# Kernel optimization log

Hardware: AMD Instinct MI355X
Metric: run time of the kernel (lower is better)

The kernel has to match this reference:

```python
import jax, jax.numpy as jnp
import numpy as np

B = 16          # number of trees (batch)
H = 256         # hidden_size == feature_size
S = 16          # Tree.num_sem
C = 5           # max_child_num (complete C-ary tree)
L = 6           # tree depth: leaves at level L, internal levels 0..L-1
N_LEAF = C**L                     # 15625
N_INT = (C**L - 1) // (C - 1)     # 3906 internal nodes, level-l offset = (C^l-1)/(C-1)


def setup_inputs() -> dict:
    key = jax.random.key(0)
    ks = jax.random.split(key, 20)
    rn = lambda k, shp, s=0.05: jax.random.normal(k, shp, dtype=jnp.float32) * s
    return {
        "leaf_box": jax.random.normal(ks[0], (B, N_LEAF, 4), dtype=jnp.float32),
        "leaf_sem": jax.random.uniform(ks[1], (B, N_LEAF, S), dtype=jnp.float32),
        "internal_box": jax.random.normal(ks[2], (B, N_INT, 4), dtype=jnp.float32),
        "node_type": jax.random.randint(ks[3], (B, N_INT), 0, 3, dtype=jnp.int32),
        "eps": jax.random.normal(ks[4], (B, H), dtype=jnp.float32),
        "W_box": rn(ks[5], (4, H)), "b_box": jnp.zeros((H,), jnp.float32),
        "W_sem": rn(ks[6], (S, H)), "b_sem": jnp.zeros((H,), jnp.float32),
        "W_node": rn(ks[7], (3, C * H, H)), "b_node": jnp.zeros((3, H), jnp.float32),
        "W1": rn(ks[8], (H, H)), "b1": jnp.zeros((H,), jnp.float32),
        "Wmu": rn(ks[9], (H, H)), "bmu": jnp.zeros((H,), jnp.float32),
        "Wvar": rn(ks[10], (H, H)), "bvar": jnp.zeros((H,), jnp.float32),
    }


def reference(leaf_box, leaf_sem, internal_box, node_type, eps,
              W_box, b_box, W_sem, b_sem, W_node, b_node,
              W1, b1, Wmu, bmu, Wvar, bvar):
    box_enc = lambda b: jax.nn.relu(b @ W_box + b_box)
    # LeafEncoder: relu-box-encoding + relu-sem-encoding
    feats = box_enc(leaf_box) + jax.nn.relu(leaf_sem @ W_sem + b_sem)  # [B, N_LEAF, H]
    # Bottom-up over internal levels (static loop over L=6 levels)
    for l in range(L - 1, -1, -1):
        n = C ** l
        off = (C ** l - 1) // (C - 1)
        child = feats.reshape(B, n, C * H)  # children flattened per parent (child_exists==1)
        # Apply all 3 branch encoders (vertical/horizontal/stack), select by node label
        y_all = jnp.einsum('bnk,tkh->bnth', child, W_node) + b_node          # [B,n,3,H]
        sel = jax.nn.one_hot(node_type[:, off:off + n], 3, dtype=child.dtype)  # [B,n,3]
        y = jnp.einsum('bnth,bnt->bnh', y_all, sel)
        feats = jax.nn.relu(y) + box_enc(internal_box[:, off:off + n])
    root = feats[:, 0]  # [B, H]
    # Sampler (variational, probabilistic)
    enc = jax.nn.relu(root @ W1 + b1)
    mu = enc @ Wmu + bmu
    logvar = enc @ Wvar + bvar
    std = jnp.exp(0.5 * logvar)
    kld = 1.0 + logvar - mu ** 2 - jnp.exp(logvar)
    return jnp.concatenate([eps * std + mu, kld], axis=1)  # [B, 2H]
```

## Files before the change

### kernel.cpp

```cpp
#include <hip/hip_runtime.h>


#define B_ 16
#define H_ 256
#define NLEAF 15625
#define NINT 3906

typedef __bf16 bf16_t;
typedef bf16_t bf16x8 __attribute__((ext_vector_type(8)));
typedef bf16_t bf16x4 __attribute__((ext_vector_type(4)));
typedef float f32x4 __attribute__((ext_vector_type(4)));

__device__ __forceinline__ void gl2lds16(const bf16_t* g, bf16_t* l) {
  __builtin_amdgcn_global_load_lds((const __attribute__((address_space(1))) void*)g,
                                   (__attribute__((address_space(3))) void*)l,
                                   16, 0, 0);
}

__global__ __launch_bounds__(256) void prep_kernel(const float* __restrict__ W_node,
                                                   bf16_t* __restrict__ Wt,
                                                   int* __restrict__ counters) {
  if (blockIdx.x == 0 && threadIdx.x < 18) counters[threadIdx.x] = 0;
  const int t = blockIdx.x / 80;
  const int kc = blockIdx.x % 80;
  const int h = threadIdx.x;
  const float* srcp = W_node + (size_t)t * 1280 * 256 + h;
  bf16_t* dstp = Wt + ((size_t)(t * 256 + h)) * 1280;
#pragma unroll
  for (int k0 = kc * 16; k0 < kc * 16 + 16; k0 += 8) {
    bf16x8 v;
#pragma unroll
    for (int j = 0; j < 8; ++j) v[j] = (bf16_t)srcp[(size_t)(k0 + j) * 256];
    *(bf16x8*)(dstp + k0) = v;
  }
}

__global__ __launch_bounds__(256) void bucket_kernel(const int* __restrict__ node_type,
                                                     int* __restrict__ counters,
                                                     int2* __restrict__ buckets) {
  __shared__ int lcnt[18];
  __shared__ int lbase[18];
  const int tid = threadIdx.x;
  if (tid < 18) lcnt[tid] = 0;
  __syncthreads();

  int idx = blockIdx.x * 256 + tid;
  bool active = idx < B_ * NINT;
  int t = 0, key = 0, mypos = 0;
  int2 e;
  int base = 0, nl_cap = 0;
  if (active) {
    int b = idx / NINT;
    int j = idx - b * NINT;
    int l, off;
    if (j >= 781)      { l = 5; off = 781; }
    else if (j >= 156) { l = 4; off = 156; }
    else if (j >= 31)  { l = 3; off = 31; }
    else if (j >= 6)   { l = 2; off = 6; }
    else if (j >= 1)   { l = 1; off = 1; }
    else               { l = 0; off = 0; }
    const int n_tab[6]    = {1, 5, 25, 125, 625, 3125};
    const int nn_tab[6]   = {5, 25, 125, 625, 3125, 15625};
    const int base_tab[6] = {0, 48, 288, 1488, 7488, 37488};
    int n_l = n_tab[l], nn = nn_tab[l];
    t = node_type[idx];
    int i = j - off;
    e.x = b * n_l + i;
    e.y = b * nn + 5 * i;
    base = base_tab[l];
    nl_cap = B_ * n_l;
    key = l * 3 + t;
    mypos = atomicAdd(&lcnt[key], 1);
  }
  __syncthreads();
  if (tid < 18) {
    int c = lcnt[tid];
    lbase[tid] = c ? atomicAdd(&counters[tid], c) : 0;
  }
  __syncthreads();
  if (active) {
    buckets[base + t * nl_cap + lbase[key] + mypos] = e;
  }
}

__global__ __launch_bounds__(256) void dest_kernel(const int2* __restrict__ buckets,
                                                   const int* __restrict__ counters,
                                                   int* __restrict__ wdest_all) {
  int flat = blockIdx.x * 256 + threadIdx.x;
  if (flat >= 187488) return;
  int l, base, cap, coff;
  if (flat >= 37488)      { l = 5; base = 37488; cap = 50000; coff = 62480; }
  else if (flat >= 7488)  { l = 4; base = 7488;  cap = 10000; coff = 12480; }
  else if (flat >= 1488)  { l = 3; base = 1488;  cap = 2000;  coff = 2480; }
  else if (flat >= 288)   { l = 2; base = 288;   cap = 400;   coff = 480; }
  else if (flat >= 48)    { l = 1; base = 48;    cap = 80;    coff = 80; }
  else                    { l = 0; base = 0;     cap = 16;    coff = 0; }
  int rel = flat - base;
  int t = (rel >= 2 * cap) ? 2 : (rel >= cap ? 1 : 0);
  int s = rel - t * cap;
  const int* c3 = counters + l * 3;
  int cnt = c3[t];
  if (s >= cnt) return;
  int pfx = (t > 0 ? c3[0] : 0) + (t > 1 ? c3[1] : 0);
  int node = buckets[flat].x;
  int grow = (pfx + s) * 5;
  int* wp = wdest_all + coff + 5 * node;
#pragma unroll
  for (int c = 0; c < 5; ++c) wp[c] = grow + c;
}

__global__ __launch_bounds__(256) void leaf_kernel(
    const float* __restrict__ leaf_box, const float* __restrict__ leaf_sem,
    const float* __restrict__ W_box, const float* __restrict__ b_box,
    const float* __restrict__ W_sem, const float* __restrict__ b_sem,
    const int* __restrict__ wd6, bf16_t* __restrict__ f6) {
  const int lane = threadIdx.x & 63;
  const int wave = threadIdx.x >> 6;
  const int q = lane >> 4;
  const int c = lane & 15;
  const int hh = wave & 1;
  const int gw = wave >> 1;

  bf16x8 wsem[8], wbox[8];
#pragma unroll
  for (int T = 0; T < 8; ++T) {
    const int hb = (hh * 8 + T) * 16 + c;
    bf16x8 a;
#pragma unroll
    for (int j = 0; j < 8; ++j) a[j] = (bf16_t)0.f;
    if (q < 2) {
#pragma unroll
      for (int j = 0; j < 8; ++j) a[j] = (bf16_t)W_sem[(q * 8 + j) * H_ + hb];
    } else if (q == 2) {
      a[0] = (bf16_t)b_sem[hb];
    }
    wsem[T] = a;
    bf16x8 b;
#pragma unroll
    for (int j = 0; j < 8; ++j) b[j] = (bf16_t)0.f;
    if (q == 0) {
#pragma unroll
      for (int j = 0; j < 4; ++j) b[j] = (bf16_t)W_box[j * H_ + hb];
      b[4] = (bf16_t)b_box[hb];
    }
    wbox[T] = b;
  }

  const int NG = (B_ * NLEAF) / 16;
  const int gstride = gridDim.x * 2;
  for (int g = blockIdx.x * 2 + gw; g < NG; g += gstride) {
    const int row = g * 16 + c;
    const int wd = wd6[row];
    bf16x8 xs, xb;
#pragma unroll
    for (int j = 0; j < 8; ++j) { xs[j] = (bf16_t)0.f; xb[j] = (bf16_t)0.f; }
    if (q < 2) {
      const float4* sp = (const float4*)(leaf_sem + (size_t)row * 16 + q * 8);
      float4 s0 = sp[0], s1 = sp[1];
      xs[0] = (bf16_t)s0.x; xs[1] = (bf16_t)s0.y; xs[2] = (bf16_t)s0.z; xs[3] = (bf16_t)s0.w;
      xs[4] = (bf16_t)s1.x; xs[5] = (bf16_t)s1.y; xs[6] = (bf16_t)s1.z; xs[7] = (bf16_t)s1.w;
    } else if (q == 2) {
      xs[0] = (bf16_t)1.0f;
    }
    if (q == 0) {
      float4 bx = *(const float4*)(leaf_box + (size_t)row * 4);
      xb[0] = (bf16_t)bx.x; xb[1] = (bf16_t)bx.y; xb[2] = (bf16_t)bx.z; xb[3] = (bf16_t)bx.w;
      xb[4] = (bf16_t)1.0f;
    }
    bf16_t* orow = f6 + (size_t)wd * H_ + hh * 128 + q * 4;
#pragma unroll
    for (int T = 0; T < 8; ++T) {
      f32x4 z = {0.f, 0.f, 0.f, 0.f};
      f32x4 as = __builtin_amdgcn_mfma_f32_16x16x32_bf16(wsem[T], xs, z, 0, 0, 0);
      f32x4 ab = __builtin_amdgcn_mfma_f32_16x16x32_bf16(wbox[T], xb, z, 0, 0, 0);
      bf16x4 o;
#pragma unroll
      for (int r = 0; r < 4; ++r)
        o[r] = (bf16_t)(fmaxf(as[r], 0.f) + fmaxf(ab[r], 0.f));
      *(bf16x4*)(orow + T * 16) = o;
    }
  }
}

__global__ __launch_bounds__(256) void level_kernel(
    const bf16_t* __restrict__ src, bf16_t* __restrict__ dst,
    const int2* __restrict__ bucket, const int* __restrict__ counters,
    const bf16_t* __restrict__ Wt, const float* __restrict__ b_node,
    const float* __restrict__ ibox, const float* __restrict__ W_box,
    const float* __restrict__ b_box, const int* __restrict__ wdest,
    int n_l, int off_l, int cap) {
  const int t = blockIdx.y;
  const int cnt = counters[t];
  const int tile0 = blockIdx.x * 128;
  if (tile0 >= cnt) return;
  const int pfx = (t > 0 ? counters[0] : 0) + (t > 1 ? counters[1] : 0);
  const int nblk = blockIdx.z;
  const int2* rd = bucket + (size_t)t * cap;

  __shared__ __align__(16) bf16_t Asm[3][128][32];
  __shared__ __align__(16) bf16_t Bsm[3][128][32];

  const int tid = threadIdx.x;
  const int lane = tid & 63;
  const int wave = tid >> 6;
  const int wm = wave & 1, wn = wave >> 1;
  const int quad = lane >> 4;
  const int l15 = lane & 15;

  const int r4 = lane >> 2;
  const int c4 = lane & 3;
  const int gch = c4 ^ ((r4 >> 1) & 3);
  const bf16_t* wsrc = Wt + ((size_t)t * 256 + nblk * 128) * 1280;
  const bf16_t* asrc = src + (size_t)pfx * 1280;
  const bf16_t* aptr[2];
  const bf16_t* bptr[2];
#pragma unroll
  for (int i = 0; i < 2; ++i) {
    int r = wave * 32 + i * 16 + r4;
    int rowi = tile0 + r;
    if (rowi >= cnt) rowi = cnt - 1;
    aptr[i] = asrc + (size_t)rowi * 1280 + gch * 8;
    bptr[i] = wsrc + (size_t)r * 1280 + gch * 8;
  }

  f32x4 acc[4][4];
#pragma unroll
  for (int i = 0; i < 4; ++i)
#pragma unroll
    for (int j = 0; j < 4; ++j) acc[i][j] = (f32x4){0.f, 0.f, 0.f, 0.f};

  const int pcs = (quad ^ ((l15 >> 1) & 3)) * 8;

#define STAGE(buf, ks)                                  \
  {                                                     \
    const int ko = (ks) * 32;                           \
    bf16_t* la = &Asm[buf][0][0] + wave * 1024;         \
    bf16_t* lb = &Bsm[buf][0][0] + wave * 1024;         \
    gl2lds16(aptr[0] + ko, la);                         \
    gl2lds16(aptr[1] + ko, la + 512);                   \
    gl2lds16(bptr[0] + ko, lb);                         \
    gl2lds16(bptr[1] + ko, lb + 512);                   \
  }

#define FRAGS_AND_MFMA(bufv)                                                  \
  {                                                                           \
    bf16x8 af[4], bfr[4];                                                     \
    _Pragma("unroll") for (int am = 0; am < 4; ++am)                          \
        af[am] = *(const bf16x8*)(&Asm[bufv][wm * 64 + am * 16 + l15][pcs]);  \
    _Pragma("unroll") for (int bn = 0; bn < 4; ++bn)                          \
        bfr[bn] = *(const bf16x8*)(&Bsm[bufv][wn * 64 + bn * 16 + l15][pcs]); \
    __builtin_amdgcn_s_setprio(1);                                            \
    _Pragma("unroll") for (int am = 0; am < 4; ++am)                          \
        _Pragma("unroll") for (int bn = 0; bn < 4; ++bn)                      \
            acc[am][bn] = __builtin_amdgcn_mfma_f32_16x16x32_bf16(            \
                af[am], bfr[bn], acc[am][bn], 0, 0, 0);                       \
    __builtin_amdgcn_s_setprio(0);                                            \
  }

  STAGE(0, 0)
  STAGE(1, 1)
  int buf = 0, nxb = 2;
  for (int ks = 0; ks < 38; ++ks) {
    asm volatile("s_waitcnt vmcnt(4)" ::: "memory");
    __builtin_amdgcn_s_barrier();
    {
      bf16x8 af[4], bfr[4];
#pragma unroll
      for (int am = 0; am < 4; ++am)
        af[am] = *(const bf16x8*)(&Asm[buf][wm * 64 + am * 16 + l15][pcs]);
#pragma unroll
      for (int bn = 0; bn < 4; ++bn)
        bfr[bn] = *(const bf16x8*)(&Bsm[buf][wn * 64 + bn * 16 + l15][pcs]);
      STAGE(nxb, ks + 2)
      __builtin_amdgcn_s_setprio(1);
#pragma unroll
      for (int am = 0; am < 4; ++am)
#pragma unroll
        for (int bn = 0; bn < 4; ++bn)
          acc[am][bn] = __builtin_amdgcn_mfma_f32_16x16x32_bf16(af[am], bfr[bn], acc[am][bn], 0, 0, 0);
      __builtin_amdgcn_s_setprio(0);
    }
    buf = (buf == 2) ? 0 : buf + 1;
    nxb = (nxb == 2) ? 0 : nxb + 1;
  }
  asm volatile("s_waitcnt vmcnt(4)" ::: "memory");
  __builtin_amdgcn_s_barrier();
  FRAGS_AND_MFMA(buf)
  buf = (buf == 2) ? 0 : buf + 1;
  asm volatile("s_waitcnt vmcnt(0)" ::: "memory");
  __builtin_amdgcn_s_barrier();
  FRAGS_AND_MFMA(buf)
#undef FRAGS_AND_MFMA
#undef STAGE

  float wbv[4][6];
#pragma unroll
  for (int bn = 0; bn < 4; ++bn) {
    int col = nblk * 128 + wn * 64 + bn * 16 + l15;
    wbv[bn][0] = W_box[col];
    wbv[bn][1] = W_box[H_ + col];
    wbv[bn][2] = W_box[2 * H_ + col];
    wbv[bn][3] = W_box[3 * H_ + col];
    wbv[bn][4] = b_box[col];
    wbv[bn][5] = b_node[t * H_ + col];
  }
#pragma unroll
  for (int am = 0; am < 4; ++am) {
    size_t obase[4]; float4 bxv[4]; bool valid[4];
#pragma unroll
    for (int r = 0; r < 4; ++r) {
      int gidx = tile0 + wm * 64 + am * 16 + quad * 4 + r;
      valid[r] = (gidx < cnt);
      int ic = valid[r] ? gidx : (cnt - 1);
      int orw = rd[ic].x;
      obase[r] = (size_t)(wdest ? wdest[orw] : orw) * H_;
      int b = orw / n_l;
      int i = orw - b * n_l;
      bxv[r] = *(const float4*)(ibox + ((size_t)b * NINT + off_l + i) * 4);
    }
#pragma unroll
    for (int bn = 0; bn < 4; ++bn) {
      int col = nblk * 128 + wn * 64 + bn * 16 + l15;
#pragma unroll
      for (int r = 0; r < 4; ++r) {
        if (!valid[r]) continue;
        float y = fmaxf(acc[am][bn][r] + wbv[bn][5], 0.f);
        float be = fmaf(wbv[bn][0], bxv[r].x,
                   fmaf(wbv[bn][1], bxv[r].y,
                   fmaf(wbv[bn][2], bxv[r].z,
                   fmaf(wbv[bn][3], bxv[r].w, wbv[bn][4]))));
        be = fmaxf(be, 0.f);
        dst[obase[r] + col] = (bf16_t)(y + be);
      }
    }
  }
}

__global__ __launch_bounds__(256) void head_kernel(
    const bf16_t* __restrict__ f0, const float* __restrict__ eps,
    const float* __restrict__ W1, const float* __restrict__ b1,
    const float* __restrict__ Wmu, const float* __restrict__ bmu,
    const float* __restrict__ Wvar, const float* __restrict__ bvar,
    float* __restrict__ out) {
  __shared__ float root[256];
  __shared__ float enc[256];
  int b = blockIdx.x, h = threadIdx.x;
  root[h] = (float)f0[b * H_ + h];
  __syncthreads();
  float a = b1[h];
  for (int k = 0; k < 256; ++k) a = fmaf(root[k], W1[k * H_ + h], a);
  enc[h] = fmaxf(a, 0.f);
  __syncthreads();
  float m = bmu[h], lv = bvar[h];
  for (int k = 0; k < 256; ++k) {
    float e = enc[k];
    m = fmaf(e, Wmu[k * H_ + h], m);
    lv = fmaf(e, Wvar[k * H_ + h], lv);
  }
  float stdv = expf(0.5f * lv);
  float kld = 1.f + lv - m * m - expf(lv);
  out[b * 512 + h] = eps[b * H_ + h] * stdv + m;
  out[b * 512 + 256 + h] = kld;
}

extern "C" void kernel_launch(void* const* d_in, const int* in_sizes, int n_in,
                              void* d_out, int out_size, void* d_ws, size_t ws_size,
                              hipStream_t stream) {
  const float* leaf_box     = (const float*)d_in[0];
  const float* leaf_sem     = (const float*)d_in[1];
  const float* internal_box = (const float*)d_in[2];
  const int*   node_type    = (const int*)d_in[3];
  const float* eps          = (const float*)d_in[4];
  const float* W_box        = (const float*)d_in[5];
  const float* b_box        = (const float*)d_in[6];
  const float* W_sem        = (const float*)d_in[7];
  const float* b_sem        = (const float*)d_in[8];
  const float* W_node       = (const float*)d_in[9];
  const float* b_node       = (const float*)d_in[10];
  const float* W1           = (const float*)d_in[11];
  const float* b1           = (const float*)d_in[12];
  const float* Wmu          = (const float*)d_in[13];
  const float* bmu          = (const float*)d_in[14];
  const float* Wvar         = (const float*)d_in[15];
  const float* bvar         = (const float*)d_in[16];
  float* out = (float*)d_out;

  char* p = (char*)d_ws;
  auto alloc = [&](size_t bytes) {
    char* r = p;
    p += (bytes + 255) & ~(size_t)255;
    return r;
  };
  bf16_t* Wt = (bf16_t*)alloc((size_t)3 * 256 * 1280 * 2);
  const int n_tab[7] = {1, 5, 25, 125, 625, 3125, 15625};
  bf16_t* f[7];
  for (int l = 0; l <= 6; ++l) f[l] = (bf16_t*)alloc((size_t)B_ * n_tab[l] * H_ * 2);
  int* counters = (int*)alloc(18 * 4);
  int2* buckets = (int2*)alloc((size_t)187488 * 8);
  int* wdest_all = (int*)alloc((size_t)312480 * 4);

  hipLaunchKernelGGL(prep_kernel, dim3(240), dim3(256), 0, stream, W_node, Wt, counters);
  hipLaunchKernelGGL(bucket_kernel, dim3((B_ * NINT + 255) / 256), dim3(256), 0, stream,
                     node_type, counters, buckets);
  hipLaunchKernelGGL(dest_kernel, dim3((187488 + 255) / 256), dim3(256), 0, stream,
                     buckets, counters, wdest_all);
  hipLaunchKernelGGL(leaf_kernel, dim3(1024), dim3(256), 0, stream,
                     leaf_box, leaf_sem, W_box, b_box, W_sem, b_sem,
                     wdest_all + 62480, f[6]);

  const int lvl_base[6] = {0, 48, 288, 1488, 7488, 37488};
  const int off_tab[6]  = {0, 1, 6, 31, 156, 781};
  const int woff[6]     = {0, 0, 80, 480, 2480, 12480};
  for (int l = 5; l >= 0; --l) {
    int cap = B_ * n_tab[l];
    int tiles = (cap + 127) / 128;
    const int* wdp = (l >= 1) ? (wdest_all + woff[l]) : nullptr;
    hipLaunchKernelGGL(level_kernel, dim3(tiles, 3, 2), dim3(256), 0, stream,
                       f[l + 1], f[l], buckets + lvl_base[l], counters + l * 3,
                       Wt, b_node, internal_box, W_box, b_box, wdp,
                       n_tab[l], off_tab[l], cap);
  }
  hipLaunchKernelGGL(head_kernel, dim3(16), dim3(256), 0, stream,
                     f[0], eps, W1, b1, Wmu, bmu, Wvar, bvar, out);
}
```

Baseline: 399.5 us.

## Store activations and weights in pre-tiled swizzled layout for contiguous LDS loads

Weights and per-level child features are written directly in a 128-row by 32-k tiled, XOR-swizzled layout, with each type segment padded to a multiple of 128 rows. The level GEMM can then stage A and B tiles with fully contiguous global-to-LDS loads, with no per-row pointer arithmetic or clamping. The leaf kernel now gathers leaves by a source index and writes straight into the tiled level-5 input. The aim is better coalescing and simpler address generation, at the cost of scattered sub-row stores in the epilogues, extra padded buffers, and more complex indexing.

New measurement: 373.5 us. 1.07x faster.

```diff
diff --git a/kernel.cpp b/kernel.cpp
--- a/kernel.cpp
+++ b/kernel.cpp
@@ -5,6 +5,7 @@
 #define H_ 256
 #define NLEAF 15625
 #define NINT 3906
+#define RND128(x) (((x) + 127) & ~127)
 
 typedef __bf16 bf16_t;
 typedef bf16_t bf16x8 __attribute__((ext_vector_type(8)));
@@ -24,14 +25,18 @@
   const int t = blockIdx.x / 80;
   const int kc = blockIdx.x % 80;
   const int h = threadIdx.x;
+  const int half = h >> 7, r = h & 127;
+  const int sw = (r >> 1) & 3;
   const float* srcp = W_node + (size_t)t * 1280 * 256 + h;
-  bf16_t* dstp = Wt + ((size_t)(t * 256 + h)) * 1280;
+  bf16_t* base = Wt + ((size_t)(t * 2 + half) * 40) * 4096 + r * 32;
 #pragma unroll
   for (int k0 = kc * 16; k0 < kc * 16 + 16; k0 += 8) {
     bf16x8 v;
 #pragma unroll
     for (int j = 0; j < 8; ++j) v[j] = (bf16_t)srcp[(size_t)(k0 + j) * 256];
-    *(bf16x8*)(dstp + k0) = v;
+    const int ks = k0 >> 5;
+    const int q = (k0 >> 3) & 3;
+    *(bf16x8*)(base + (size_t)ks * 4096 + ((q ^ sw) << 3)) = v;
   }
 }
 
@@ -85,11 +90,12 @@
 
 __global__ __launch_bounds__(256) void dest_kernel(const int2* __restrict__ buckets,
                                                    const int* __restrict__ counters,
-                                                   int* __restrict__ wdest_all) {
+                                                   int* __restrict__ wdest_all,
+                                                   int* __restrict__ rsrc6) {
   int flat = blockIdx.x * 256 + threadIdx.x;
   if (flat >= 187488) return;
   int l, base, cap, coff;
-  if (flat >= 37488)      { l = 5; base = 37488; cap = 50000; coff = 62480; }
+  if (flat >= 37488)      { l = 5; base = 37488; cap = 50000; coff = 0; }
   else if (flat >= 7488)  { l = 4; base = 7488;  cap = 10000; coff = 12480; }
   else if (flat >= 1488)  { l = 3; base = 1488;  cap = 2000;  coff = 2480; }
   else if (flat >= 288)   { l = 2; base = 288;   cap = 400;   coff = 480; }
@@ -99,21 +105,26 @@
   int t = (rel >= 2 * cap) ? 2 : (rel >= cap ? 1 : 0);
   int s = rel - t * cap;
   const int* c3 = counters + l * 3;
-  int cnt = c3[t];
-  if (s >= cnt) return;
-  int pfx = (t > 0 ? c3[0] : 0) + (t > 1 ? c3[1] : 0);
-  int node = buckets[flat].x;
-  int grow = (pfx + s) * 5;
-  int* wp = wdest_all + coff + 5 * node;
-#pragma unroll
-  for (int c = 0; c < 5; ++c) wp[c] = grow + c;
+  if (s >= c3[t]) return;
+  int pfxr = (t > 0 ? RND128(c3[0]) : 0) + (t > 1 ? RND128(c3[1]) : 0);
+  int R = pfxr + s;
+  int2 e = buckets[flat];
+  if (l == 5) {
+    int* rp = rsrc6 + 5 * R;
+#pragma unroll
+    for (int c = 0; c < 5; ++c) rp[c] = e.y + c;
+  } else {
+    int* wp = wdest_all + coff + 5 * e.x;
+#pragma unroll
+    for (int c = 0; c < 5; ++c) wp[c] = (R << 3) + c;
+  }
 }
 
 __global__ __launch_bounds__(256) void leaf_kernel(
     const float* __restrict__ leaf_box, const float* __restrict__ leaf_sem,
     const float* __restrict__ W_box, const float* __restrict__ b_box,
     const float* __restrict__ W_sem, const float* __restrict__ b_sem,
-    const int* __restrict__ wd6, bf16_t* __restrict__ f6) {
+    const int* __restrict__ rsrc, bf16_t* __restrict__ g5) {
   const int lane = threadIdx.x & 63;
   const int wave = threadIdx.x >> 6;
   const int q = lane >> 4;
@@ -146,11 +157,14 @@
     wbox[T] = b;
   }
 
-  const int NG = (B_ * NLEAF) / 16;
+  const int NG2 = 15705;
   const int gstride = gridDim.x * 2;
-  for (int g = blockIdx.x * 2 + gw; g < NG; g += gstride) {
-    const int row = g * 16 + c;
-    const int wd = wd6[row];
+  for (int g = blockIdx.x * 2 + gw; g < NG2; g += gstride) {
+    const int ci = g * 16 + c;
+    int row = rsrc[ci];
+    row = ((unsigned)row < (unsigned)(B_ * NLEAF)) ? row : 0;
+    const int R = ci / 5;
+    const int c5 = ci - R * 5;
     bf16x8 xs, xb;
 #pragma unroll
     for (int j = 0; j < 8; ++j) { xs[j] = (bf16_t)0.f; xb[j] = (bf16_t)0.f; }
@@ -167,7 +181,9 @@
       xb[0] = (bf16_t)bx.x; xb[1] = (bf16_t)bx.y; xb[2] = (bf16_t)bx.z; xb[3] = (bf16_t)bx.w;
       xb[4] = (bf16_t)1.0f;
     }
-    bf16_t* orow = f6 + (size_t)wd * H_ + hh * 128 + q * 4;
+    const int rr = R & 127;
+    const int sw = (rr >> 1) & 3;
+    bf16_t* obase = g5 + (size_t)(R >> 7) * 163840 + rr * 32;
 #pragma unroll
     for (int T = 0; T < 8; ++T) {
       f32x4 z = {0.f, 0.f, 0.f, 0.f};
@@ -177,7 +193,9 @@
 #pragma unroll
       for (int r = 0; r < 4; ++r)
         o[r] = (bf16_t)(fmaxf(as[r], 0.f) + fmaxf(ab[r], 0.f));
-      *(bf16x4*)(orow + T * 16) = o;
+      const int ks = c5 * 8 + hh * 4 + (T >> 1);
+      const int pc = (((T & 1) << 1) | (q >> 1)) ^ sw;
+      *(bf16x4*)(obase + (size_t)ks * 4096 + (pc << 3) + ((q & 1) << 2)) = o;
     }
   }
 }
@@ -193,7 +211,7 @@
   const int cnt = counters[t];
   const int tile0 = blockIdx.x * 128;
   if (tile0 >= cnt) return;
-  const int pfx = (t > 0 ? counters[0] : 0) + (t > 1 ? counters[1] : 0);
+  const int pfxr = (t > 0 ? RND128(counters[0]) : 0) + (t > 1 ? RND128(counters[1]) : 0);
   const int nblk = blockIdx.z;
   const int2* rd = bucket + (size_t)t * cap;
 
@@ -207,21 +225,8 @@
   const int quad = lane >> 4;
   const int l15 = lane & 15;
 
-  const int r4 = lane >> 2;
-  const int c4 = lane & 3;
-  const int gch = c4 ^ ((r4 >> 1) & 3);
-  const bf16_t* wsrc = Wt + ((size_t)t * 256 + nblk * 128) * 1280;
-  const bf16_t* asrc = src + (size_t)pfx * 1280;
-  const bf16_t* aptr[2];
-  const bf16_t* bptr[2];
-#pragma unroll
-  for (int i = 0; i < 2; ++i) {
-    int r = wave * 32 + i * 16 + r4;
-    int rowi = tile0 + r;
-    if (rowi >= cnt) rowi = cnt - 1;
-    aptr[i] = asrc + (size_t)rowi * 1280 + gch * 8;
-    bptr[i] = wsrc + (size_t)r * 1280 + gch * 8;
-  }
+  const bf16_t* ga0 = src + (size_t)(pfxr + tile0) * 1280 + wave * 1024 + (lane << 3);
+  const bf16_t* gb0 = Wt + ((size_t)(t * 2 + nblk) * 40) * 4096 + wave * 1024 + (lane << 3);
 
   f32x4 acc[4][4];
 #pragma unroll
@@ -233,13 +238,14 @@
 
 #define STAGE(buf, ks)                                  \
   {                                                     \
-    const int ko = (ks) * 32;                           \
+    const bf16_t* ga = ga0 + (ks) * 4096;               \
+    const bf16_t* gb = gb0 + (ks) * 4096;               \
     bf16_t* la = &Asm[buf][0][0] + wave * 1024;         \
     bf16_t* lb = &Bsm[buf][0][0] + wave * 1024;         \
-    gl2lds16(aptr[0] + ko, la);                         \
-    gl2lds16(aptr[1] + ko, la + 512);                   \
-    gl2lds16(bptr[0] + ko, lb);                         \
-    gl2lds16(bptr[1] + ko, lb + 512);                   \
+    gl2lds16(ga, la);                                   \
+    gl2lds16(ga + 512, la + 512);                       \
+    gl2lds16(gb, lb);                                   \
+    gl2lds16(gb + 512, lb + 512);                       \
   }
 
 #define FRAGS_AND_MFMA(bufv)                                                  \
@@ -306,31 +312,59 @@
   }
 #pragma unroll
   for (int am = 0; am < 4; ++am) {
-    size_t obase[4]; float4 bxv[4]; bool valid[4];
+    int orw_[4]; float4 bxv[4]; bool valid[4];
 #pragma unroll
     for (int r = 0; r < 4; ++r) {
       int gidx = tile0 + wm * 64 + am * 16 + quad * 4 + r;
       valid[r] = (gidx < cnt);
       int ic = valid[r] ? gidx : (cnt - 1);
       int orw = rd[ic].x;
-      obase[r] = (size_t)(wdest ? wdest[orw] : orw) * H_;
+      orw_[r] = orw;
       int b = orw / n_l;
       int i = orw - b * n_l;
       bxv[r] = *(const float4*)(ibox + ((size_t)b * NINT + off_l + i) * 4);
     }
-#pragma unroll
-    for (int bn = 0; bn < 4; ++bn) {
-      int col = nblk * 128 + wn * 64 + bn * 16 + l15;
+    if (wdest) {
+      size_t ob[4]; int sw_[4];
 #pragma unroll
       for (int r = 0; r < 4; ++r) {
-        if (!valid[r]) continue;
-        float y = fmaxf(acc[am][bn][r] + wbv[bn][5], 0.f);
-        float be = fmaf(wbv[bn][0], bxv[r].x,
-                   fmaf(wbv[bn][1], bxv[r].y,
-                   fmaf(wbv[bn][2], bxv[r].z,
-                   fmaf(wbv[bn][3], bxv[r].w, wbv[bn][4]))));
-        be = fmaxf(be, 0.f);
-        dst[obase[r] + col] = (bf16_t)(y + be);
+        int wd = wdest[orw_[r]];
+        int R = wd >> 3, cc = wd & 7;
+        int rr = R & 127;
+        ob[r] = (size_t)(R >> 7) * 163840 + (size_t)cc * 32768 + (size_t)rr * 32;
+        sw_[r] = (rr >> 1) & 3;
+      }
+#pragma unroll
+      for (int bn = 0; bn < 4; ++bn) {
+        int col = nblk * 128 + wn * 64 + bn * 16 + l15;
+        int kc2 = col >> 5, qq = (col >> 3) & 3, ww = col & 7;
+#pragma unroll
+        for (int r = 0; r < 4; ++r) {
+          if (!valid[r]) continue;
+          float y = fmaxf(acc[am][bn][r] + wbv[bn][5], 0.f);
+          float be = fmaf(wbv[bn][0], bxv[r].x,
+                     fmaf(wbv[bn][1], bxv[r].y,
+                     fmaf(wbv[bn][2], bxv[r].z,
+                     fmaf(wbv[bn][3], bxv[r].w, wbv[bn][4]))));
+          be = fmaxf(be, 0.f);
+          dst[ob[r] + (size_t)kc2 * 4096 + ((qq ^ sw_[r]) << 3) + ww] = (bf16_t)(y + be);
+        }
+      }
+    } else {
+#pragma unroll
+      for (int bn = 0; bn < 4; ++bn) {
+        int col = nblk * 128 + wn * 64 + bn * 16 + l15;
+#pragma unroll
+        for (int r = 0; r < 4; ++r) {
+          if (!valid[r]) continue;
+          float y = fmaxf(acc[am][bn][r] + wbv[bn][5], 0.f);
+          float be = fmaf(wbv[bn][0], bxv[r].x,
+                     fmaf(wbv[bn][1], bxv[r].y,
+                     fmaf(wbv[bn][2], bxv[r].z,
+                     fmaf(wbv[bn][3], bxv[r].w, wbv[bn][4]))));
+          be = fmaxf(be, 0.f);
+          dst[(size_t)orw_[r] * H_ + col] = (bf16_t)(y + be);
+        }
       }
     }
   }
@@ -391,22 +425,24 @@
     p += (bytes + 255) & ~(size_t)255;
     return r;
   };
-  bf16_t* Wt = (bf16_t*)alloc((size_t)3 * 256 * 1280 * 2);
-  const int n_tab[7] = {1, 5, 25, 125, 625, 3125, 15625};
-  bf16_t* f[7];
-  for (int l = 0; l <= 6; ++l) f[l] = (bf16_t*)alloc((size_t)B_ * n_tab[l] * H_ * 2);
-  int* counters = (int*)alloc(18 * 4);
-  int2* buckets = (int2*)alloc((size_t)187488 * 8);
-  int* wdest_all = (int*)alloc((size_t)312480 * 4);
+  const int n_tab[6] = {1, 5, 25, 125, 625, 3125};
+  bf16_t* Wt = (bf16_t*)alloc((size_t)3 * 2 * 40 * 4096 * 2);
+  bf16_t* f0 = (bf16_t*)alloc((size_t)B_ * H_ * 2);
+  bf16_t* G[6];
+  for (int l = 0; l <= 5; ++l)
+    G[l] = (bf16_t*)alloc(((size_t)B_ * n_tab[l] + 384) * 1280 * 2);
+  int* counters  = (int*)alloc(18 * 4);
+  int2* buckets  = (int2*)alloc((size_t)187488 * 8);
+  int* wdest_all = (int*)alloc((size_t)62480 * 4);
+  int* rsrc6     = (int*)alloc((size_t)251280 * 4);
 
   hipLaunchKernelGGL(prep_kernel, dim3(240), dim3(256), 0, stream, W_node, Wt, counters);
   hipLaunchKernelGGL(bucket_kernel, dim3((B_ * NINT + 255) / 256), dim3(256), 0, stream,
                      node_type, counters, buckets);
   hipLaunchKernelGGL(dest_kernel, dim3((187488 + 255) / 256), dim3(256), 0, stream,
-                     buckets, counters, wdest_all);
+                     buckets, counters, wdest_all, rsrc6);
   hipLaunchKernelGGL(leaf_kernel, dim3(1024), dim3(256), 0, stream,
-                     leaf_box, leaf_sem, W_box, b_box, W_sem, b_sem,
-                     wdest_all + 62480, f[6]);
+                     leaf_box, leaf_sem, W_box, b_box, W_sem, b_sem, rsrc6, G[5]);
 
   const int lvl_base[6] = {0, 48, 288, 1488, 7488, 37488};
   const int off_tab[6]  = {0, 1, 6, 31, 156, 781};
@@ -416,10 +452,10 @@
     int tiles = (cap + 127) / 128;
     const int* wdp = (l >= 1) ? (wdest_all + woff[l]) : nullptr;
     hipLaunchKernelGGL(level_kernel, dim3(tiles, 3, 2), dim3(256), 0, stream,
-                       f[l + 1], f[l], buckets + lvl_base[l], counters + l * 3,
-                       Wt, b_node, internal_box, W_box, b_box, wdp,
-                       n_tab[l], off_tab[l], cap);
+                       G[l], (l >= 1) ? G[l - 1] : f0, buckets + lvl_base[l],
+                       counters + l * 3, Wt, b_node, internal_box, W_box, b_box,
+                       wdp, n_tab[l], off_tab[l], cap);
   }
   hipLaunchKernelGGL(head_kernel, dim3(16), dim3(256), 0, stream,
-                     f[0], eps, W1, b1, Wmu, bmu, Wvar, bvar, out);
-}
+                     f0, eps, W1, b1, Wmu, bmu, Wvar, bvar, out);
+}
```
